# Kernel tuning notes

Hardware: AMD Instinct MI355X
Metric: run time of the kernel (lower is better)

The kernel has to match this reference:

```python
import jax, jax.numpy as jnp
import numpy as np

MAP_SIZE = 56
K_STEEP = 10.0  # boxcar sigmoid steepness (the 'k=10' default in the original)


def setup_inputs() -> dict:
    key = jax.random.key(0)
    k1, k2, k3 = jax.random.split(key, 3)
    B, D, H = 16384, 1024, 512
    x = jax.random.normal(k1, (B, D), dtype=jnp.float32)
    W1 = jax.random.normal(k2, (D, H), dtype=jnp.float32) * (1.0 / np.sqrt(D))
    b1 = jnp.zeros((H,), dtype=jnp.float32)
    W2 = jax.random.normal(k3, (H, 3), dtype=jnp.float32) * (1.0 / np.sqrt(H))
    b2 = jnp.zeros((3,), dtype=jnp.float32)
    return {"x": x, "W1": W1, "b1": b1, "W2": W2, "b2": b2}


def boxcar(t, map_size=MAP_SIZE, k=K_STEEP):
    # t: [B, 3] = (x_center, y_center, size). Vectorized over batch and grid.
    t0 = t[:, 0][:, None, None]  # [B,1,1]
    t1 = t[:, 1][:, None, None]
    t2 = t[:, 2][:, None, None]
    i = jnp.arange(map_size, dtype=t.dtype)[None, :, None]  # [1,S,1]
    j = jnp.arange(map_size, dtype=t.dtype)[None, None, :]  # [1,1,S]
    Vx = jax.nn.sigmoid(k * (i - t0 + 0.5 * t2)) - jax.nn.sigmoid(k * (i - t0 - 0.5 * t2))
    Vy = jax.nn.sigmoid(k * (j - t1 + 0.5 * t2)) - jax.nn.sigmoid(k * (j - t1 - 0.5 * t2))
    return Vx * Vy  # [B,S,S]


def reference(x, W1, b1, W2, b2):
    # fc1 -> fc2 (flatten output is discarded in the original call(), as in source)
    h = x @ W1 + b1          # [B, hidden]
    t = h @ W2 + b2          # [B, 3]
    return boxcar(t)         # [B, map_size, map_size]
```

## Files before the change

### kernel.cpp

```cpp
#include <hip/hip_runtime.h>
#include <math.h>

#define MAP 56
#define KST 10.0f
#define BATCH 16384
#define DIM 1024
#define HID 512
#define RPB 8
#define RPW 4

__global__ __launch_bounds__(64) void fold_weights(
    const float* __restrict__ W1, const float* __restrict__ b1,
    const float* __restrict__ W2, const float* __restrict__ b2,
    float* __restrict__ WeffT, float* __restrict__ beff)
{
    const int d = blockIdx.x;
    const int lane = threadIdx.x;
    const float* row = (d < DIM) ? (W1 + (size_t)d * HID) : b1;

    float a0 = 0.f, a1 = 0.f, a2 = 0.f;
    for (int h = lane; h < HID; h += 64) {
        const float w = row[h];
        a0 += w * W2[h * 3 + 0];
        a1 += w * W2[h * 3 + 1];
        a2 += w * W2[h * 3 + 2];
    }
    #pragma unroll
    for (int off = 32; off; off >>= 1) {
        a0 += __shfl_down(a0, off, 64);
        a1 += __shfl_down(a1, off, 64);
        a2 += __shfl_down(a2, off, 64);
    }
    if (lane == 0) {
        if (d < DIM) {
            WeffT[0 * DIM + d] = a0;
            WeffT[1 * DIM + d] = a1;
            WeffT[2 * DIM + d] = a2;
        } else {
            beff[0] = a0 + b2[0];
            beff[1] = a1 + b2[1];
            beff[2] = a2 + b2[2];
        }
    }
}

__global__ __launch_bounds__(256) void gemv_kernel(
    const float* __restrict__ x, const float* __restrict__ WeffT,
    const float* __restrict__ beff, float4* __restrict__ t4)
{
    const int tid  = threadIdx.x;
    const int wave = tid >> 6;
    const int lane = tid & 63;
    const int row0 = blockIdx.x * (4 * RPW) + wave * RPW;

    float4 wf[3][4];
    #pragma unroll
    for (int q = 0; q < 4; ++q)
        #pragma unroll
        for (int c = 0; c < 3; ++c)
            wf[c][q] = *(const float4*)(WeffT + c * DIM + 4 * lane + 256 * q);

    float acc[RPW][3];
    #pragma unroll
    for (int r = 0; r < RPW; ++r) { acc[r][0] = acc[r][1] = acc[r][2] = 0.f; }

    #pragma unroll
    for (int r = 0; r < RPW; ++r) {
        const float* xr = x + (size_t)(row0 + r) * DIM;
        #pragma unroll
        for (int q = 0; q < 4; ++q) {
            const float4 xv = *(const float4*)(xr + 4 * lane + 256 * q);
            acc[r][0] += xv.x * wf[0][q].x + xv.y * wf[0][q].y + xv.z * wf[0][q].z + xv.w * wf[0][q].w;
            acc[r][1] += xv.x * wf[1][q].x + xv.y * wf[1][q].y + xv.z * wf[1][q].z + xv.w * wf[1][q].w;
            acc[r][2] += xv.x * wf[2][q].x + xv.y * wf[2][q].y + xv.z * wf[2][q].z + xv.w * wf[2][q].w;
        }
    }
    #pragma unroll
    for (int off = 32; off; off >>= 1)
        #pragma unroll
        for (int r = 0; r < RPW; ++r) {
            acc[r][0] += __shfl_down(acc[r][0], off, 64);
            acc[r][1] += __shfl_down(acc[r][1], off, 64);
            acc[r][2] += __shfl_down(acc[r][2], off, 64);
        }
    if (lane == 0) {
        const float b0 = beff[0], b1 = beff[1], b2 = beff[2];
        #pragma unroll
        for (int r = 0; r < RPW; ++r)
            t4[row0 + r] = make_float4(acc[r][0] + b0, acc[r][1] + b1, acc[r][2] + b2, 0.f);
    }
}

__global__ __launch_bounds__(256) void boxcar_kernel(
    const float4* __restrict__ t4, float* __restrict__ out)
{
    __shared__ float  sVx[RPB][MAP];
    __shared__ float4 sVy4[RPB][MAP / 4];

    const int tid  = threadIdx.x;
    const int base = blockIdx.x * RPB;

    for (int e = tid; e < RPB * 2 * MAP; e += 256) {
        const int sub = e / (2 * MAP);
        const int ent = e - sub * (2 * MAP);
        const float4 t = t4[base + sub];
        const int  isY = ent >= MAP;
        const int  i   = isY ? ent - MAP : ent;
        const float tc = isY ? t.y : t.x;
        const float u  = (float)i - tc;
        const float hh = 0.5f * t.z;
        const float p  = 1.0f / (1.0f + __expf(-KST * (u + hh)));
        const float m  = 1.0f / (1.0f + __expf(-KST * (u - hh)));
        const float v  = p - m;
        if (isY) ((float*)&sVy4[sub][0])[i] = v;
        else     sVx[sub][i] = v;
    }
    __syncthreads();

    float4* ob = (float4*)(out + (size_t)base * (MAP * MAP));
    for (int g = tid; g < RPB * (MAP * MAP / 4); g += 256) {
        const int sub = g / (MAP * MAP / 4);
        const int rem = g - sub * (MAP * MAP / 4);
        const int i   = rem / (MAP / 4);
        const int jq  = rem - i * (MAP / 4);
        const float  vx = sVx[sub][i];
        const float4 vy = sVy4[sub][jq];
        ob[g] = make_float4(vx * vy.x, vx * vy.y, vx * vy.z, vx * vy.w);
    }
}

extern "C" void kernel_launch(void* const* d_in, const int* in_sizes, int n_in,
                              void* d_out, int out_size, void* d_ws, size_t ws_size,
                              hipStream_t stream) {
    const float* x  = (const float*)d_in[0];
    const float* W1 = (const float*)d_in[1];
    const float* b1 = (const float*)d_in[2];
    const float* W2 = (const float*)d_in[3];
    const float* b2 = (const float*)d_in[4];
    float* out = (float*)d_out;

    float*  WeffT = (float*)d_ws;
    float*  beff  = WeffT + 3 * DIM;
    float4* t4    = (float4*)(beff + 4);

    fold_weights<<<DIM + 1, 64, 0, stream>>>(W1, b1, W2, b2, WeffT, beff);
    gemv_kernel<<<BATCH / (4 * RPW), 256, 0, stream>>>(x, WeffT, beff, t4);
    boxcar_kernel<<<BATCH / RPB, 256, 0, stream>>>(t4, out);
}
```

Measured before the change: 273.1 us.

## Fuse GEMV and boxcar into one kernel with nontemporal loads and stores

Merges the projection GEMV and the boxcar map generation into a single kernel. Each block computes the 3-vector for its 8 rows into shared memory and then writes the 56x56 maps, which removes one launch and the round trip of t through global memory. It also switches x loads and output stores to nontemporal builtins to reduce cache pollution on streaming traffic. The cost is that each block now serialises its GEMV phase before its write phase, with fewer rows per wave than before.

```diff
diff --git a/kernel.cpp b/kernel.cpp
--- a/kernel.cpp
+++ b/kernel.cpp
@@ -7,7 +7,8 @@
 #define DIM 1024
 #define HID 512
 #define RPB 8
-#define RPW 4
+
+typedef float floatx4 __attribute__((ext_vector_type(4)));
 
 __global__ __launch_bounds__(64) void fold_weights(
     const float* __restrict__ W1, const float* __restrict__ b1,
@@ -44,71 +45,66 @@
     }
 }
 
-__global__ __launch_bounds__(256) void gemv_kernel(
+__global__ __launch_bounds__(256) void fused_kernel(
     const float* __restrict__ x, const float* __restrict__ WeffT,
-    const float* __restrict__ beff, float4* __restrict__ t4)
+    const float* __restrict__ beff, float* __restrict__ out)
 {
+    __shared__ float   sVx[RPB][MAP];
+    __shared__ floatx4 sVy4[RPB][MAP / 4];
+    __shared__ float   st[RPB][4];
+
     const int tid  = threadIdx.x;
     const int wave = tid >> 6;
     const int lane = tid & 63;
-    const int row0 = blockIdx.x * (4 * RPW) + wave * RPW;
+    const int base = blockIdx.x * RPB;
 
-    float4 wf[3][4];
+    const float* xr0 = x + (size_t)(base + 2 * wave + 0) * DIM + 4 * lane;
+    const float* xr1 = x + (size_t)(base + 2 * wave + 1) * DIM + 4 * lane;
+    float a00 = 0.f, a01 = 0.f, a02 = 0.f;
+    float a10 = 0.f, a11 = 0.f, a12 = 0.f;
     #pragma unroll
-    for (int q = 0; q < 4; ++q)
-        #pragma unroll
-        for (int c = 0; c < 3; ++c)
-            wf[c][q] = *(const float4*)(WeffT + c * DIM + 4 * lane + 256 * q);
-
-    float acc[RPW][3];
-    #pragma unroll
-    for (int r = 0; r < RPW; ++r) { acc[r][0] = acc[r][1] = acc[r][2] = 0.f; }
-
-    #pragma unroll
-    for (int r = 0; r < RPW; ++r) {
-        const float* xr = x + (size_t)(row0 + r) * DIM;
-        #pragma unroll
-        for (int q = 0; q < 4; ++q) {
-            const float4 xv = *(const float4*)(xr + 4 * lane + 256 * q);
-            acc[r][0] += xv.x * wf[0][q].x + xv.y * wf[0][q].y + xv.z * wf[0][q].z + xv.w * wf[0][q].w;
-            acc[r][1] += xv.x * wf[1][q].x + xv.y * wf[1][q].y + xv.z * wf[1][q].z + xv.w * wf[1][q].w;
-            acc[r][2] += xv.x * wf[2][q].x + xv.y * wf[2][q].y + xv.z * wf[2][q].z + xv.w * wf[2][q].w;
-        }
+    for (int q = 0; q < 4; ++q) {
+        const int off = 256 * q;
+        const floatx4 w0 = *(const floatx4*)(WeffT + 0 * DIM + 4 * lane + off);
+        const floatx4 w1 = *(const floatx4*)(WeffT + 1 * DIM + 4 * lane + off);
+        const floatx4 w2 = *(const floatx4*)(WeffT + 2 * DIM + 4 * lane + off);
+        const floatx4 x0 = __builtin_nontemporal_load((const floatx4*)(xr0 + off));
+        const floatx4 x1 = __builtin_nontemporal_load((const floatx4*)(xr1 + off));
+        a00 += x0.x * w0.x + x0.y * w0.y + x0.z * w0.z + x0.w * w0.w;
+        a01 += x0.x * w1.x + x0.y * w1.y + x0.z * w1.z + x0.w * w1.w;
+        a02 += x0.x * w2.x + x0.y * w2.y + x0.z * w2.z + x0.w * w2.w;
+        a10 += x1.x * w0.x + x1.y * w0.y + x1.z * w0.z + x1.w * w0.w;
+        a11 += x1.x * w1.x + x1.y * w1.y + x1.z * w1.z + x1.w * w1.w;
+        a12 += x1.x * w2.x + x1.y * w2.y + x1.z * w2.z + x1.w * w2.w;
     }
     #pragma unroll
-    for (int off = 32; off; off >>= 1)
-        #pragma unroll
-        for (int r = 0; r < RPW; ++r) {
-            acc[r][0] += __shfl_down(acc[r][0], off, 64);
-            acc[r][1] += __shfl_down(acc[r][1], off, 64);
-            acc[r][2] += __shfl_down(acc[r][2], off, 64);
-        }
+    for (int off = 32; off; off >>= 1) {
+        a00 += __shfl_down(a00, off, 64);
+        a01 += __shfl_down(a01, off, 64);
+        a02 += __shfl_down(a02, off, 64);
+        a10 += __shfl_down(a10, off, 64);
+        a11 += __shfl_down(a11, off, 64);
+        a12 += __shfl_down(a12, off, 64);
+    }
     if (lane == 0) {
         const float b0 = beff[0], b1 = beff[1], b2 = beff[2];
-        #pragma unroll
-        for (int r = 0; r < RPW; ++r)
-            t4[row0 + r] = make_float4(acc[r][0] + b0, acc[r][1] + b1, acc[r][2] + b2, 0.f);
+        st[2 * wave + 0][0] = a00 + b0;
+        st[2 * wave + 0][1] = a01 + b1;
+        st[2 * wave + 0][2] = a02 + b2;
+        st[2 * wave + 1][0] = a10 + b0;
+        st[2 * wave + 1][1] = a11 + b1;
+        st[2 * wave + 1][2] = a12 + b2;
     }
-}
-
-__global__ __launch_bounds__(256) void boxcar_kernel(
-    const float4* __restrict__ t4, float* __restrict__ out)
-{
-    __shared__ float  sVx[RPB][MAP];
-    __shared__ float4 sVy4[RPB][MAP / 4];
-
-    const int tid  = threadIdx.x;
-    const int base = blockIdx.x * RPB;
+    __syncthreads();
 
     for (int e = tid; e < RPB * 2 * MAP; e += 256) {
         const int sub = e / (2 * MAP);
         const int ent = e - sub * (2 * MAP);
-        const float4 t = t4[base + sub];
-        const int  isY = ent >= MAP;
-        const int  i   = isY ? ent - MAP : ent;
-        const float tc = isY ? t.y : t.x;
+        const int isY = ent >= MAP;
+        const int i   = isY ? ent - MAP : ent;
+        const float tc = isY ? st[sub][1] : st[sub][0];
         const float u  = (float)i - tc;
-        const float hh = 0.5f * t.z;
+        const float hh = 0.5f * st[sub][2];
         const float p  = 1.0f / (1.0f + __expf(-KST * (u + hh)));
         const float m  = 1.0f / (1.0f + __expf(-KST * (u - hh)));
         const float v  = p - m;
@@ -117,15 +113,17 @@
     }
     __syncthreads();
 
-    float4* ob = (float4*)(out + (size_t)base * (MAP * MAP));
+    floatx4* ob = (floatx4*)(out + (size_t)base * (MAP * MAP));
     for (int g = tid; g < RPB * (MAP * MAP / 4); g += 256) {
         const int sub = g / (MAP * MAP / 4);
         const int rem = g - sub * (MAP * MAP / 4);
         const int i   = rem / (MAP / 4);
         const int jq  = rem - i * (MAP / 4);
-        const float  vx = sVx[sub][i];
-        const float4 vy = sVy4[sub][jq];
-        ob[g] = make_float4(vx * vy.x, vx * vy.y, vx * vy.z, vx * vy.w);
+        const float   vx = sVx[sub][i];
+        const floatx4 vy = sVy4[sub][jq];
+        floatx4 o;
+        o.x = vx * vy.x; o.y = vx * vy.y; o.z = vx * vy.z; o.w = vx * vy.w;
+        __builtin_nontemporal_store(o, &ob[g]);
     }
 }
 
@@ -139,11 +137,9 @@
     const float* b2 = (const float*)d_in[4];
     float* out = (float*)d_out;
 
-    float*  WeffT = (float*)d_ws;
-    float*  beff  = WeffT + 3 * DIM;
-    float4* t4    = (float4*)(beff + 4);
+    float* WeffT = (float*)d_ws;
+    float* beff  = WeffT + 3 * DIM;
 
     fold_weights<<<DIM + 1, 64, 0, stream>>>(W1, b1, W2, b2, WeffT, beff);
-    gemv_kernel<<<BATCH / (4 * RPW), 256, 0, stream>>>(x, WeffT, beff, t4);
-    boxcar_kernel<<<BATCH / RPB, 256, 0, stream>>>(t4, out);
+    fused_kernel<<<BATCH / RPB, 256, 0, stream>>>(x, WeffT, beff, out);
 }
```

New measurement: 262.7 us. 1.04x faster.
